# Performance work log

Hardware: AMD Instinct MI355X
Metric: run time of the kernel (lower is better)

## Reference

```python
import jax, jax.numpy as jnp
import numpy as np

EPS = 1e-5

def conv2d(x, w, b=None, pad=1):
    # x: [B,C,H,W], w: [O,I,kh,kw]
    y = jax.lax.conv_general_dilated(x, w, (1, 1), [(pad, pad), (pad, pad)],
                                     dimension_numbers=('NCHW', 'OIHW', 'NCHW'))
    if b is not None:
        y = y + b[None, :, None, None]
    return y

def bn(x, g, b, m, v):
    # inference-mode batchnorm
    inv = g / jnp.sqrt(v + EPS)
    return x * inv[None, :, None, None] + (b - m * inv)[None, :, None, None]

def coord_conv(x, w, b):
    B, C, H, W = x.shape
    yy = jnp.broadcast_to(jnp.linspace(-1.0, 1.0, H)[:, None], (H, W))
    xx = jnp.broadcast_to(jnp.linspace(-1.0, 1.0, W)[None, :], (H, W))
    coords = jnp.broadcast_to(jnp.stack([xx, yy])[None], (B, 2, H, W)).astype(x.dtype)
    return conv2d(jnp.concatenate([x, coords], axis=1), w, b, pad=1)

def deform_conv(x, offset, w):
    # deformable conv v1, 3x3, pad=1, stride=1, no bias
    B, C, H, W = x.shape
    K = 9
    # offset channels interleaved (y, x) per kernel tap
    off = offset.reshape(B, K, 2, H, W)
    off_y, off_x = off[:, :, 0], off[:, :, 1]          # [B,9,H,W]
    k = jnp.arange(K)
    ko_y = (k // 3 - 1).astype(x.dtype)[None, :, None, None]
    ko_x = (k % 3 - 1).astype(x.dtype)[None, :, None, None]
    base_y = jnp.arange(H, dtype=x.dtype)[None, None, :, None]
    base_x = jnp.arange(W, dtype=x.dtype)[None, None, None, :]
    py = base_y + ko_y + off_y                          # [B,9,H,W]
    px = base_x + ko_x + off_x
    xf = x.reshape(B, C, H * W)
    y0 = jnp.floor(py)
    x0 = jnp.floor(px)
    acc = jnp.zeros((B, C, K, H, W), x.dtype)
    for dy in (0.0, 1.0):
        for dx in (0.0, 1.0):
            yy = y0 + dy
            xx = x0 + dx
            wgt = (1.0 - jnp.abs(py - yy)) * (1.0 - jnp.abs(px - xx))
            valid = (yy >= 0) & (yy < H) & (xx >= 0) & (xx < W)
            wgt = jnp.where(valid, wgt, 0.0)            # zero padding OOB
            yi = jnp.clip(yy, 0, H - 1).astype(jnp.int32)
            xi = jnp.clip(xx, 0, W - 1).astype(jnp.int32)
            idx = (yi * W + xi).reshape(B, K * H * W)
            v = jnp.take_along_axis(xf, idx[:, None, :], axis=2).reshape(B, C, K, H, W)
            acc = acc + v * wgt[:, None]
    wk = w.reshape(w.shape[0], w.shape[1], K)           # [O,I,9]
    return jnp.einsum('bckhw,ock->bohw', acc, wk)

def setup_inputs() -> dict:
    key = jax.random.key(0)
    ks = jax.random.split(key, 16)
    d_model, hd = 256, 64
    B, H, W = 8, 96, 96
    f32 = jnp.float32
    def bn_params(k):
        k1, k2, k3 = jax.random.split(k, 3)
        return (1.0 + 0.1 * jax.random.normal(k1, (hd,), f32),
                0.1 * jax.random.normal(k2, (hd,), f32),
                0.1 * jax.random.normal(k3, (hd,), f32),
                0.5 + jax.random.uniform(jax.random.fold_in(k, 7), (hd,), f32))
    bn1 = bn_params(ks[1]); bn2 = bn_params(ks[2]); bn3 = bn_params(ks[3]); bn4 = bn_params(ks[4])
    inp = {
        'features': jax.random.normal(ks[0], (B, H, W, d_model), f32),
        'coord_w': 0.05 * jax.random.normal(ks[5], (hd, d_model + 2, 3, 3), f32),
        'coord_b': jnp.zeros((hd,), f32),
        'bn1_g': bn1[0], 'bn1_b': bn1[1], 'bn1_m': bn1[2], 'bn1_v': bn1[3],
        'off_w': 0.01 * jax.random.normal(ks[6], (18, hd, 3, 3), f32),
        'off_b': 0.01 * jax.random.normal(ks[7], (18,), f32),
        'dc_w': 0.05 * jax.random.normal(ks[8], (hd, hd, 3, 3), f32),
        'bn2_g': bn2[0], 'bn2_b': bn2[1], 'bn2_m': bn2[2], 'bn2_v': bn2[3],
        'r1_w': 0.05 * jax.random.normal(ks[9], (hd, hd, 3, 3), f32),
        'bn3_g': bn3[0], 'bn3_b': bn3[1], 'bn3_m': bn3[2], 'bn3_v': bn3[3],
        'r2_w': 0.05 * jax.random.normal(ks[10], (hd, hd, 3, 3), f32),
        'bn4_g': bn4[0], 'bn4_b': bn4[1], 'bn4_m': bn4[2], 'bn4_v': bn4[3],
        'out_w': 0.1 * jax.random.normal(ks[11], (1, hd, 1, 1), f32),
        'out_b': jnp.zeros((1,), f32),
    }
    return inp

def reference(features, coord_w, coord_b, bn1_g, bn1_b, bn1_m, bn1_v,
              off_w, off_b, dc_w, bn2_g, bn2_b, bn2_m, bn2_v,
              r1_w, bn3_g, bn3_b, bn3_m, bn3_v,
              r2_w, bn4_g, bn4_b, bn4_m, bn4_v, out_w, out_b):
    x = jnp.transpose(features, (0, 3, 1, 2))           # NHWC -> NCHW
    x = jax.nn.relu(bn(coord_conv(x, coord_w, coord_b), bn1_g, bn1_b, bn1_m, bn1_v))
    offset = conv2d(x, off_w, off_b, pad=1)
    x = deform_conv(x, offset, dc_w)
    x = jax.nn.relu(bn(x, bn2_g, bn2_b, bn2_m, bn2_v))
    x = jax.nn.relu(bn(conv2d(x, r1_w, None, pad=1), bn3_g, bn3_b, bn3_m, bn3_v))
    x = jax.nn.relu(bn(conv2d(x, r2_w, None, pad=1), bn4_g, bn4_b, bn4_m, bn4_v))
    return jax.nn.sigmoid(conv2d(x, out_w, out_b, pad=0))
```

## Files before the change

### kernel.cpp

```cpp
#include <hip/hip_runtime.h>


typedef unsigned short u16;
typedef unsigned int u32;
typedef __attribute__((ext_vector_type(8)))  short bf16x8;
typedef __attribute__((ext_vector_type(16))) float f32x16;

#define EPSBN 1e-5f

__device__ __forceinline__ u16 f2bf(float f) {
  u32 u = __builtin_bit_cast(u32, f);
  u32 r = u + 0x7FFFu + ((u >> 16) & 1u);
  return (u16)(r >> 16);
}
__device__ __forceinline__ u32 pk2(float a, float b) {
  return (u32)f2bf(a) | ((u32)f2bf(b) << 16);
}
__device__ __forceinline__ float lo2f(u32 w) { return __builtin_bit_cast(float, w << 16); }
__device__ __forceinline__ float hi2f(u32 w) { return __builtin_bit_cast(float, w & 0xFFFF0000u); }

#define N_WCF 147456
#define N_WCC 9216
#define N_WOF 18432
#define N_W64 36864
#define N_ALLW (N_WCF + N_WCC + N_WOF + 3*N_W64)

__global__ __launch_bounds__(256) void prep_kernel(
    const float* __restrict__ coord_w, const float* __restrict__ off_w,
    const float* __restrict__ dc_w, const float* __restrict__ r1_w,
    const float* __restrict__ r2_w,
    u16* __restrict__ wcf, u16* __restrict__ wcc, u16* __restrict__ wof,
    u16* __restrict__ wdf, u16* __restrict__ wr1, u16* __restrict__ wr2)
{
  int i = blockIdx.x * 256 + threadIdx.x;
  if (i >= N_ALLW) return;
  int d = i;
  if (d < N_WCF) {
    int j = d & 7, lane = (d >> 3) & 63, frag = d >> 9;
    int nt = frag & 1, h = (frag >> 1) & 3, tap = (frag >> 3) % 9, cc = (frag >> 3) / 9;
    int ic = cc * 64 + h * 16 + ((lane >> 5) << 3) + j;
    int oc = nt * 32 + (lane & 31);
    wcf[d] = f2bf(coord_w[((size_t)oc * 258 + ic) * 9 + tap]);
    return;
  }
  d -= N_WCF;
  if (d < N_WCC) {
    int j = d & 7, lane = (d >> 3) & 63, frag = d >> 9;
    int nt = frag & 1, tap = frag >> 1;
    int ic = 256 + ((lane >> 5) << 3) + j;
    int oc = nt * 32 + (lane & 31);
    wcc[d] = (ic < 258) ? f2bf(coord_w[((size_t)oc * 258 + ic) * 9 + tap]) : (u16)0;
    return;
  }
  d -= N_WCC;
  if (d < N_WOF) {
    int j = d & 7, lane = (d >> 3) & 63, frag = d >> 9;
    int h = frag & 3, tap = frag >> 2;
    int ic = h * 16 + ((lane >> 5) << 3) + j;
    int oc = lane & 31;
    wof[d] = (oc < 18) ? f2bf(off_w[((size_t)oc * 64 + ic) * 9 + tap]) : (u16)0;
    return;
  }
  d -= N_WOF;
  int seg = d / N_W64;
  int e = d - seg * N_W64;
  int j = e & 7, lane = (e >> 3) & 63, frag = e >> 9;
  int nt = frag & 1, h = (frag >> 1) & 3, tap = frag >> 3;
  int ic = h * 16 + ((lane >> 5) << 3) + j;
  int oc = nt * 32 + (lane & 31);
  const float* src = (seg == 0) ? dc_w : (seg == 1) ? r1_w : r2_w;
  u16* dst = (seg == 0) ? wdf : (seg == 1) ? wr1 : wr2;
  dst[e] = f2bf(src[((size_t)oc * 64 + ic) * 9 + tap]);
}

__global__ __launch_bounds__(512, 2) void coord_conv_kernel(
    const float* __restrict__ feat, const u16* __restrict__ wcf,
    const u16* __restrict__ wcc, const float* __restrict__ cb,
    const float* __restrict__ g, const float* __restrict__ bb,
    const float* __restrict__ m, const float* __restrict__ v,
    u16* __restrict__ x1b)
{
  __shared__ __align__(16) u16 tile[6 * 34 * 72];
  const int t = threadIdx.x;
  const int wv = t >> 6, lane = t & 63;
  const int l31 = lane & 31, l5 = lane >> 5;
  const int rp = wv & 1, ntw = (wv >> 1) & 1, kh = wv >> 2;
  const int x0 = blockIdx.x * 32, y0 = blockIdx.y * 4, b = blockIdx.z;

  f32x16 acc[2] = {};
  float4 pa[4], pb[4];
  bf16x8 wfr[18];

  auto issueF = [&](int cc) {
    #pragma unroll
    for (int r = 0; r < 4; ++r) {
      const int i = t + r * 512;
      const float4 z = {0.f, 0.f, 0.f, 0.f};
      pa[r] = z; pb[r] = z;
      if (i < 1632) {
        const int px = i >> 3, gg = i & 7;
        const int ly = px / 34, lx = px - ly * 34;
        const int gy = y0 + ly - 1, gx = x0 + lx - 1;
        if ((unsigned)gy < 96u && (unsigned)gx < 96u) {
          const float* p = feat + ((size_t)((b * 96 + gy) * 96 + gx)) * 256
                           + cc * 64 + gg * 8;
          pa[r] = *(const float4*)p;
          pb[r] = *(const float4*)(p + 4);
        }
      }
    }
  };
  auto commitF = [&]() {
    #pragma unroll
    for (int r = 0; r < 4; ++r) {
      const int i = t + r * 512;
      if (i < 1632) {
        const int px = i >> 3, gg = i & 7;
        uint4 o;
        o.x = pk2(pa[r].x, pa[r].y); o.y = pk2(pa[r].z, pa[r].w);
        o.z = pk2(pb[r].x, pb[r].y); o.w = pk2(pb[r].z, pb[r].w);
        *(uint4*)(tile + px * 72 + gg * 8) = o;
      }
    }
  };
  auto loadW = [&](int cc) {
    #pragma unroll
    for (int tap = 0; tap < 9; ++tap)
      #pragma unroll
      for (int hh = 0; hh < 2; ++hh) {
        const int h = kh * 2 + hh;
        wfr[tap * 2 + hh] = *(const bf16x8*)(wcf +
            ((size_t)((((cc * 9 + tap) * 4 + h) * 2) + ntw)) * 512 + lane * 8);
      }
  };

  issueF(0);
  loadW(0);
  for (int cc = 0; cc < 4; ++cc) {
    __syncthreads();
    commitF();
    __syncthreads();
    if (cc < 3) issueF(cc + 1);
    #pragma unroll
    for (int tap = 0; tap < 9; ++tap) {
      const int dy = tap / 3, dx = tap - dy * 3;
      #pragma unroll
      for (int hh = 0; hh < 2; ++hh) {
        const bf16x8 bfr = wfr[tap * 2 + hh];
        #pragma unroll
        for (int ai = 0; ai < 2; ++ai) {
          const bf16x8 afr = *(const bf16x8*)(tile +
              ((rp * 2 + ai + dy) * 34 + l31 + dx) * 72
              + (kh * 2 + hh) * 16 + l5 * 8);
          acc[ai] = __builtin_amdgcn_mfma_f32_32x32x16_bf16(afr, bfr, acc[ai],
                                                            0, 0, 0);
        }
      }
    }
    if (cc < 3) loadW(cc + 1);
  }

  bf16x8 wcr[9];
  if (kh == 0) {
    #pragma unroll
    for (int tap = 0; tap < 9; ++tap)
      wcr[tap] = *(const bf16x8*)(wcc + ((size_t)(tap * 2 + ntw)) * 512
                                  + lane * 8);
  }
  __syncthreads();
  for (int i = t; i < 408; i += 512) {
    const int px = i >> 1, gg = i & 1;
    const int ly = px / 34, lx = px - ly * 34;
    const int gy = y0 + ly - 1, gx = x0 + lx - 1;
    uint4 o = {0u, 0u, 0u, 0u};
    if (gg == 0 && (unsigned)gy < 96u && (unsigned)gx < 96u) {
      const float xx = -1.f + (2.f / 95.f) * (float)gx;
      const float yy = -1.f + (2.f / 95.f) * (float)gy;
      o.x = pk2(xx, yy);
    }
    *(uint4*)(tile + (ly * 34 + lx) * 72 + gg * 8) = o;
  }
  __syncthreads();
  if (kh == 0) {
    #pragma unroll
    for (int tap = 0; tap < 9; ++tap) {
      const int dy = tap / 3, dx = tap - dy * 3;
      #pragma unroll
      for (int ai = 0; ai < 2; ++ai) {
        const bf16x8 afr = *(const bf16x8*)(tile +
            ((rp * 2 + ai + dy) * 34 + l31 + dx) * 72 + l5 * 8);
        acc[ai] = __builtin_amdgcn_mfma_f32_32x32x16_bf16(afr, wcr[tap],
                                                          acc[ai], 0, 0, 0);
      }
    }
  }

  float* redk = (float*)tile;
  const int slot = wv & 3;
  #pragma unroll
  for (int ai = 0; ai < 2; ++ai) {
    __syncthreads();
    if (kh == 1) {
      #pragma unroll
      for (int r = 0; r < 16; ++r)
        redk[(r * 4 + slot) * 64 + lane] = acc[ai][r];
    }
    __syncthreads();
    if (kh == 0) {
      #pragma unroll
      for (int r = 0; r < 16; ++r)
        acc[ai][r] += redk[(r * 4 + slot) * 64 + lane];
    }
  }

  if (kh == 0) {
    const int oc = ntw * 32 + l31;
    const float inv = g[oc] * rsqrtf(v[oc] + EPSBN);
    const float sh = bb[oc] - m[oc] * inv + cb[oc] * inv;
    #pragma unroll
    for (int ai = 0; ai < 2; ++ai) {
      const int y = y0 + rp * 2 + ai;
      #pragma unroll
      for (int r = 0; r < 16; ++r) {
        const int xr = (r & 3) + 8 * (r >> 2) + 4 * l5;
        const float val = fmaxf(fmaf(acc[ai][r], inv, sh), 0.f);
        x1b[((size_t)((b * 96 + y) * 96 + x0 + xr)) * 64 + oc] = f2bf(val);
      }
    }
  }
}

template<int NN, int EPI>
__global__ __launch_bounds__(512, 2) void conv64_kernel(
    const u16* __restrict__ xin, const u16* __restrict__ wf,
    const float* __restrict__ bias,
    const float* __restrict__ g, const float* __restrict__ bb,
    const float* __restrict__ m, const float* __restrict__ v,
    const float* __restrict__ ow, const float* __restrict__ ob,
    void* __restrict__ outp)
{
  __shared__ __align__(16) u16 tile[6 * 34 * 72];
  __shared__ float red2[2][128];
  const int t = threadIdx.x;
  const int wv = t >> 6, lane = t & 63;
  const int l31 = lane & 31, l5 = lane >> 5;
  const int rp  = (NN == 2) ? (wv & 1) : 0;
  const int ntw = (NN == 2) ? ((wv >> 1) & 1) : 0;
  const int row = (NN == 2) ? 0 : (wv & 3);
  const int kh  = wv >> 2;
  const int x0 = blockIdx.x * 32, y0 = blockIdx.y * 4, b = blockIdx.z;

  uint4 pf[4];
  #pragma unroll
  for (int r = 0; r < 4; ++r) {
    const int i = t + r * 512;
    const uint4 z = {0u, 0u, 0u, 0u};
    pf[r] = z;
    if (i < 1632) {
      const int px = i >> 3, gg = i & 7;
      const int ly = px / 34, lx = px - ly * 34;
      const int gy = y0 + ly - 1, gx = x0 + lx - 1;
      if ((unsigned)gy < 96u && (unsigned)gx < 96u)
        pf[r] = *(const uint4*)(xin + (((size_t)((b * 96 + gy) * 96 + gx)) << 6)
                                + gg * 8);
    }
  }
  bf16x8 wfr[18];
  #pragma unroll
  for (int tap = 0; tap < 9; ++tap)
    #pragma unroll
    for (int hh = 0; hh < 2; ++hh) {
      const int h = kh * 2 + hh;
      const size_t f = (NN == 2) ? (size_t)((tap * 4 + h) * 2 + ntw)
                                 : (size_t)(tap * 4 + h);
      wfr[tap * 2 + hh] = *(const bf16x8*)(wf + f * 512 + lane * 8);
    }
  #pragma unroll
  for (int r = 0; r < 4; ++r) {
    const int i = t + r * 512;
    if (i < 1632) {
      const int px = i >> 3, gg = i & 7;
      *(uint4*)(tile + px * 72 + gg * 8) = pf[r];
    }
  }
  __syncthreads();

  constexpr int NA = (NN == 2) ? 2 : 1;
  f32x16 acc[NA] = {};
  #pragma unroll
  for (int tap = 0; tap < 9; ++tap) {
    const int dy = tap / 3, dx = tap - dy * 3;
    #pragma unroll
    for (int hh = 0; hh < 2; ++hh) {
      const int h = kh * 2 + hh;
      #pragma unroll
      for (int ai = 0; ai < NA; ++ai) {
        const int rr = (NN == 2) ? (rp * 2 + ai) : row;
        const bf16x8 afr = *(const bf16x8*)(tile +
            ((rr + dy) * 34 + l31 + dx) * 72 + h * 16 + l5 * 8);
        acc[ai] = __builtin_amdgcn_mfma_f32_32x32x16_bf16(afr, wfr[tap * 2 + hh],
                                                          acc[ai], 0, 0, 0);
      }
    }
  }

  float* redk = (float*)tile;
  const int slot = (NN == 2) ? (wv & 3) : row;
  #pragma unroll
  for (int ai = 0; ai < NA; ++ai) {
    __syncthreads();
    if (kh == 1) {
      #pragma unroll
      for (int r = 0; r < 16; ++r)
        redk[(r * 4 + slot) * 64 + lane] = acc[ai][r];
    }
    __syncthreads();
    if (kh == 0) {
      #pragma unroll
      for (int r = 0; r < 16; ++r)
        acc[ai][r] += redk[(r * 4 + slot) * 64 + lane];
    }
  }

  if constexpr (EPI == 0) {
    if (kh == 0) {
      u16* xo = (u16*)outp;
      const int oc = ntw * 32 + l31;
      const float inv = g[oc] * rsqrtf(v[oc] + EPSBN);
      const float sh = bb[oc] - m[oc] * inv;
      #pragma unroll
      for (int ai = 0; ai < NA; ++ai) {
        const int y = y0 + rp * 2 + ai;
        #pragma unroll
        for (int r = 0; r < 16; ++r) {
          const int xr = (r & 3) + 8 * (r >> 2) + 4 * l5;
          const float val = fmaxf(fmaf(acc[ai][r], inv, sh), 0.f);
          xo[((size_t)((b * 96 + y) * 96 + x0 + xr)) * 64 + oc] = f2bf(val);
        }
      }
    }
  } else if constexpr (EPI == 1) {
    if (kh == 0 && l31 < 18) {
      float* fo = (float*)outp;
      const int y = y0 + row;
      const float bs = bias[l31];
      #pragma unroll
      for (int r = 0; r < 16; ++r) {
        const int xr = (r & 3) + 8 * (r >> 2) + 4 * l5;
        fo[((size_t)((b * 96 + y) * 96 + x0 + xr)) * 18 + l31] = acc[0][r] + bs;
      }
    }
  } else {
    if (kh == 0) {
      const int oc = ntw * 32 + l31;
      const float inv = g[oc] * rsqrtf(v[oc] + EPSBN);
      const float sh = bb[oc] - m[oc] * inv;
      const float wo = ow[oc];
      #pragma unroll
      for (int ai = 0; ai < NA; ++ai) {
        float pr[16];
        #pragma unroll
        for (int r = 0; r < 16; ++r) {
          const float val = fmaxf(fmaf(acc[ai][r], inv, sh), 0.f);
          pr[r] = val * wo;
        }
        #pragma unroll
        for (int mask = 1; mask <= 16; mask <<= 1)
          #pragma unroll
          for (int r = 0; r < 16; ++r)
            pr[r] += __shfl_xor(pr[r], mask);
        if (l31 == 0) {
          #pragma unroll
          for (int r = 0; r < 16; ++r) {
            const int xr = (r & 3) + 8 * (r >> 2) + 4 * l5;
            red2[ntw][(rp * 2 + ai) * 32 + xr] = pr[r];
          }
        }
      }
    }
    __syncthreads();
    if (t < 128) {
      float* fo = (float*)outp;
      const int yy = y0 + (t >> 5), xx = x0 + (t & 31);
      const float val = red2[0][t] + red2[1][t] + ob[0];
      fo[(size_t)(b * 96 + yy) * 96 + xx] = 1.f / (1.f + expf(-val));
    }
  }
}

__global__ __launch_bounds__(512, 4) void deform_kernel(
    const u16* __restrict__ x1b, const float* __restrict__ off,
    const u16* __restrict__ wdf,
    const float* __restrict__ g, const float* __restrict__ bb,
    const float* __restrict__ m, const float* __restrict__ v,
    u16* __restrict__ x2b)
{
  __shared__ __align__(16) u16 s[2 * 128 * 72];
  __shared__ float offs[128 * 18];
  const int t = threadIdx.x;
  const int wv = t >> 6, lane = t & 63;
  const int l31 = lane & 31, l5 = lane >> 5;
  const int mt = wv & 3, ntw = wv >> 2;
  const int x0 = blockIdx.x * 16, y0 = blockIdx.y * 8, b = blockIdx.z;

  {
    float po[5];
    #pragma unroll
    for (int r = 0; r < 5; ++r) {
      const int i = t + r * 512;
      po[r] = 0.f;
      if (i < 2304) {
        const int p = i / 18, c = i - p * 18;
        const int gy = y0 + (p >> 4), gx = x0 + (p & 15);
        po[r] = off[((size_t)((b * 96 + gy) * 96 + gx)) * 18 + c];
      }
    }
    #pragma unroll
    for (int r = 0; r < 5; ++r) {
      const int i = t + r * 512;
      if (i < 2304) offs[i] = po[r];
    }
  }
  __syncthreads();

  const int sp = t >> 2, part = t & 3;
  const int sy = y0 + (sp >> 4), sx = x0 + (sp & 15);

  uint4 gbuf[8];
  float w4[4];

  auto prefetch = [&](int k) {
    const float oy = offs[sp * 18 + 2 * k];
    const float ox = offs[sp * 18 + 2 * k + 1];
    const float py = (float)(sy + k / 3 - 1) + oy;
    const float px = (float)(sx + k % 3 - 1) + ox;
    const float yf = floorf(py), xf = floorf(px);
    const float fy = py - yf, fx = px - xf;
    const int yi = (int)yf, xi = (int)xf;
    #pragma unroll
    for (int cor = 0; cor < 4; ++cor) {
      const int cy = yi + (cor >> 1), cx = xi + (cor & 1);
      const uint4 z = {0u, 0u, 0u, 0u};
      gbuf[2 * cor] = z; gbuf[2 * cor + 1] = z;
      const float wy = (cor & 2) ? fy : 1.f - fy;
      const float wx = (cor & 1) ? fx : 1.f - fx;
      w4[cor] = 0.f;
      if ((unsigned)cy < 96u && (unsigned)cx < 96u) {
        w4[cor] = wy * wx;
        const u16* p = x1b + ((size_t)((b * 96 + cy) * 96 + cx)) * 64
                       + part * 16;
        gbuf[2 * cor]     = *(const uint4*)p;
        gbuf[2 * cor + 1] = *(const uint4*)(p + 8);
      }
    }
  };
  auto combine = [&](u16* dst) {
    float val[16];
    #pragma unroll
    for (int j = 0; j < 16; ++j) val[j] = 0.f;
    #pragma unroll
    for (int cor = 0; cor < 4; ++cor) {
      const float wgt = w4[cor];
      const u32 uu[8] = {gbuf[2 * cor].x, gbuf[2 * cor].y,
                         gbuf[2 * cor].z, gbuf[2 * cor].w,
                         gbuf[2 * cor + 1].x, gbuf[2 * cor + 1].y,
                         gbuf[2 * cor + 1].z, gbuf[2 * cor + 1].w};
      #pragma unroll
      for (int u = 0; u < 8; ++u) {
        val[2 * u]     = fmaf(wgt, lo2f(uu[u]), val[2 * u]);
        val[2 * u + 1] = fmaf(wgt, hi2f(uu[u]), val[2 * u + 1]);
      }
    }
    u32 pk[8];
    #pragma unroll
    for (int u = 0; u < 8; ++u) pk[u] = pk2(val[2 * u], val[2 * u + 1]);
    uint4 w0 = {pk[0], pk[1], pk[2], pk[3]};
    uint4 w1 = {pk[4], pk[5], pk[6], pk[7]};
    *(uint4*)(dst + sp * 72 + part * 16) = w0;
    *(uint4*)(dst + sp * 72 + part * 16 + 8) = w1;
  };

  f32x16 acc = {};

  prefetch(0);
  combine(s);
  __syncthreads();

  for (int k = 0; k < 9; ++k) {
    u16* cur = s + (k & 1) * 9216;
    if (k < 8) prefetch(k + 1);
    #pragma unroll
    for (int h = 0; h < 4; ++h) {
      const bf16x8 afr = *(const bf16x8*)(cur + (mt * 32 + l31) * 72
                                          + h * 16 + l5 * 8);
      const bf16x8 bfr = *(const bf16x8*)(wdf +
          ((size_t)((k * 4 + h) * 2 + ntw)) * 512 + lane * 8);
      acc = __builtin_amdgcn_mfma_f32_32x32x16_bf16(afr, bfr, acc, 0, 0, 0);
    }
    if (k < 8) combine(s + ((k + 1) & 1) * 9216);
    __syncthreads();
  }

  const int oc = ntw * 32 + l31;
  const float inv = g[oc] * rsqrtf(v[oc] + EPSBN);
  const float sh = bb[oc] - m[oc] * inv;
  #pragma unroll
  for (int r = 0; r < 16; ++r) {
    const int pxi = mt * 32 + (r & 3) + 8 * (r >> 2) + 4 * l5;
    const int y = y0 + (pxi >> 4), x = x0 + (pxi & 15);
    const float val = fmaxf(fmaf(acc[r], inv, sh), 0.f);
    x2b[((size_t)((b * 96 + y) * 96 + x)) * 64 + oc] = f2bf(val);
  }
}

extern "C" void kernel_launch(void* const* d_in, const int* in_sizes, int n_in,
                              void* d_out, int out_size, void* d_ws,
                              size_t ws_size, hipStream_t stream)
{
  (void)in_sizes; (void)n_in; (void)out_size; (void)ws_size;
  const float* features = (const float*)d_in[0];
  const float* coord_w  = (const float*)d_in[1];
  const float* coord_b  = (const float*)d_in[2];
  const float* bn1g = (const float*)d_in[3];
  const float* bn1b = (const float*)d_in[4];
  const float* bn1m = (const float*)d_in[5];
  const float* bn1v = (const float*)d_in[6];
  const float* off_w = (const float*)d_in[7];
  const float* off_b = (const float*)d_in[8];
  const float* dc_w  = (const float*)d_in[9];
  const float* bn2g = (const float*)d_in[10];
  const float* bn2b = (const float*)d_in[11];
  const float* bn2m = (const float*)d_in[12];
  const float* bn2v = (const float*)d_in[13];
  const float* r1_w = (const float*)d_in[14];
  const float* bn3g = (const float*)d_in[15];
  const float* bn3b = (const float*)d_in[16];
  const float* bn3m = (const float*)d_in[17];
  const float* bn3v = (const float*)d_in[18];
  const float* r2_w = (const float*)d_in[19];
  const float* bn4g = (const float*)d_in[20];
  const float* bn4b = (const float*)d_in[21];
  const float* bn4m = (const float*)d_in[22];
  const float* bn4v = (const float*)d_in[23];
  const float* out_w = (const float*)d_in[24];
  const float* out_b = (const float*)d_in[25];

  char* W = (char*)d_ws;
  float* offb = (float*)W;
  u16*   x1b  = (u16*)(W + 5308416);
  u16*   x2b  = (u16*)(W + 14745600);
  u16*   x3b  = (u16*)(W + 24182784);
  u16*   wcf  = (u16*)(W + 33619968);
  u16*   wcc  = wcf + N_WCF;
  u16*   wof  = wcc + N_WCC;
  u16*   wdf  = wof + N_WOF;
  u16*   wr1  = wdf + N_W64;
  u16*   wr2  = wr1 + N_W64;

  prep_kernel<<<(N_ALLW + 255) / 256, 256, 0, stream>>>(
      coord_w, off_w, dc_w, r1_w, r2_w, wcf, wcc, wof, wdf, wr1, wr2);

  dim3 grid(3, 24, 8);
  dim3 gridD(6, 12, 8);

  coord_conv_kernel<<<grid, 512, 0, stream>>>(
      features, wcf, wcc, coord_b, bn1g, bn1b, bn1m, bn1v, x1b);
  conv64_kernel<1, 1><<<grid, 512, 0, stream>>>(
      x1b, wof, off_b, nullptr, nullptr, nullptr, nullptr, nullptr, nullptr,
      (void*)offb);
  deform_kernel<<<gridD, 512, 0, stream>>>(
      x1b, offb, wdf, bn2g, bn2b, bn2m, bn2v, x2b);
  conv64_kernel<2, 0><<<grid, 512, 0, stream>>>(
      x2b, wr1, nullptr, bn3g, bn3b, bn3m, bn3v, nullptr, nullptr, (void*)x3b);
  conv64_kernel<2, 2><<<grid, 512, 0, stream>>>(
      x3b, wr2, nullptr, bn4g, bn4b, bn4m, bn4v, out_w, out_b, d_out);
}
```

Baseline: 251.0 us.

## Fuse offset conv into deform kernel and fuse the two residual convs

The offset conv is now computed inside the deformable-conv kernel from a haloed x1 tile in shared memory, so the fp32 offset tensor is never written to or read from global memory. The two trailing 3x3 convs plus the 1x1 sigmoid head are merged into one kernel that recomputes the first conv over a halo region and keeps the intermediate in LDS, which drops the x3 round trip and two launches. In exchange, halo pixels are computed redundantly, LDS use per block rises (which may lower occupancy), and the deform kernel's launch bound drops from 4 to 2 blocks.

```diff
diff --git a/kernel.cpp b/kernel.cpp
--- a/kernel.cpp
+++ b/kernel.cpp
@@ -230,199 +230,95 @@
   }
 }
 
-template<int NN, int EPI>
-__global__ __launch_bounds__(512, 2) void conv64_kernel(
-    const u16* __restrict__ xin, const u16* __restrict__ wf,
-    const float* __restrict__ bias,
-    const float* __restrict__ g, const float* __restrict__ bb,
-    const float* __restrict__ m, const float* __restrict__ v,
-    const float* __restrict__ ow, const float* __restrict__ ob,
-    void* __restrict__ outp)
-{
-  __shared__ __align__(16) u16 tile[6 * 34 * 72];
-  __shared__ float red2[2][128];
-  const int t = threadIdx.x;
-  const int wv = t >> 6, lane = t & 63;
-  const int l31 = lane & 31, l5 = lane >> 5;
-  const int rp  = (NN == 2) ? (wv & 1) : 0;
-  const int ntw = (NN == 2) ? ((wv >> 1) & 1) : 0;
-  const int row = (NN == 2) ? 0 : (wv & 3);
-  const int kh  = wv >> 2;
-  const int x0 = blockIdx.x * 32, y0 = blockIdx.y * 4, b = blockIdx.z;
-
-  uint4 pf[4];
-  #pragma unroll
-  for (int r = 0; r < 4; ++r) {
-    const int i = t + r * 512;
-    const uint4 z = {0u, 0u, 0u, 0u};
-    pf[r] = z;
-    if (i < 1632) {
-      const int px = i >> 3, gg = i & 7;
-      const int ly = px / 34, lx = px - ly * 34;
-      const int gy = y0 + ly - 1, gx = x0 + lx - 1;
-      if ((unsigned)gy < 96u && (unsigned)gx < 96u)
-        pf[r] = *(const uint4*)(xin + (((size_t)((b * 96 + gy) * 96 + gx)) << 6)
-                                + gg * 8);
-    }
-  }
-  bf16x8 wfr[18];
-  #pragma unroll
-  for (int tap = 0; tap < 9; ++tap)
-    #pragma unroll
-    for (int hh = 0; hh < 2; ++hh) {
-      const int h = kh * 2 + hh;
-      const size_t f = (NN == 2) ? (size_t)((tap * 4 + h) * 2 + ntw)
-                                 : (size_t)(tap * 4 + h);
-      wfr[tap * 2 + hh] = *(const bf16x8*)(wf + f * 512 + lane * 8);
-    }
-  #pragma unroll
-  for (int r = 0; r < 4; ++r) {
-    const int i = t + r * 512;
-    if (i < 1632) {
-      const int px = i >> 3, gg = i & 7;
-      *(uint4*)(tile + px * 72 + gg * 8) = pf[r];
-    }
-  }
-  __syncthreads();
-
-  constexpr int NA = (NN == 2) ? 2 : 1;
-  f32x16 acc[NA] = {};
-  #pragma unroll
-  for (int tap = 0; tap < 9; ++tap) {
-    const int dy = tap / 3, dx = tap - dy * 3;
-    #pragma unroll
-    for (int hh = 0; hh < 2; ++hh) {
-      const int h = kh * 2 + hh;
-      #pragma unroll
-      for (int ai = 0; ai < NA; ++ai) {
-        const int rr = (NN == 2) ? (rp * 2 + ai) : row;
-        const bf16x8 afr = *(const bf16x8*)(tile +
-            ((rr + dy) * 34 + l31 + dx) * 72 + h * 16 + l5 * 8);
-        acc[ai] = __builtin_amdgcn_mfma_f32_32x32x16_bf16(afr, wfr[tap * 2 + hh],
-                                                          acc[ai], 0, 0, 0);
-      }
-    }
-  }
-
-  float* redk = (float*)tile;
-  const int slot = (NN == 2) ? (wv & 3) : row;
-  #pragma unroll
-  for (int ai = 0; ai < NA; ++ai) {
-    __syncthreads();
-    if (kh == 1) {
-      #pragma unroll
-      for (int r = 0; r < 16; ++r)
-        redk[(r * 4 + slot) * 64 + lane] = acc[ai][r];
-    }
-    __syncthreads();
-    if (kh == 0) {
-      #pragma unroll
-      for (int r = 0; r < 16; ++r)
-        acc[ai][r] += redk[(r * 4 + slot) * 64 + lane];
-    }
-  }
-
-  if constexpr (EPI == 0) {
-    if (kh == 0) {
-      u16* xo = (u16*)outp;
-      const int oc = ntw * 32 + l31;
-      const float inv = g[oc] * rsqrtf(v[oc] + EPSBN);
-      const float sh = bb[oc] - m[oc] * inv;
-      #pragma unroll
-      for (int ai = 0; ai < NA; ++ai) {
-        const int y = y0 + rp * 2 + ai;
-        #pragma unroll
-        for (int r = 0; r < 16; ++r) {
-          const int xr = (r & 3) + 8 * (r >> 2) + 4 * l5;
-          const float val = fmaxf(fmaf(acc[ai][r], inv, sh), 0.f);
-          xo[((size_t)((b * 96 + y) * 96 + x0 + xr)) * 64 + oc] = f2bf(val);
-        }
-      }
-    }
-  } else if constexpr (EPI == 1) {
-    if (kh == 0 && l31 < 18) {
-      float* fo = (float*)outp;
-      const int y = y0 + row;
-      const float bs = bias[l31];
-      #pragma unroll
-      for (int r = 0; r < 16; ++r) {
-        const int xr = (r & 3) + 8 * (r >> 2) + 4 * l5;
-        fo[((size_t)((b * 96 + y) * 96 + x0 + xr)) * 18 + l31] = acc[0][r] + bs;
-      }
-    }
-  } else {
-    if (kh == 0) {
-      const int oc = ntw * 32 + l31;
-      const float inv = g[oc] * rsqrtf(v[oc] + EPSBN);
-      const float sh = bb[oc] - m[oc] * inv;
-      const float wo = ow[oc];
-      #pragma unroll
-      for (int ai = 0; ai < NA; ++ai) {
-        float pr[16];
-        #pragma unroll
-        for (int r = 0; r < 16; ++r) {
-          const float val = fmaxf(fmaf(acc[ai][r], inv, sh), 0.f);
-          pr[r] = val * wo;
-        }
-        #pragma unroll
-        for (int mask = 1; mask <= 16; mask <<= 1)
-          #pragma unroll
-          for (int r = 0; r < 16; ++r)
-            pr[r] += __shfl_xor(pr[r], mask);
-        if (l31 == 0) {
-          #pragma unroll
-          for (int r = 0; r < 16; ++r) {
-            const int xr = (r & 3) + 8 * (r >> 2) + 4 * l5;
-            red2[ntw][(rp * 2 + ai) * 32 + xr] = pr[r];
-          }
-        }
-      }
-    }
-    __syncthreads();
-    if (t < 128) {
-      float* fo = (float*)outp;
-      const int yy = y0 + (t >> 5), xx = x0 + (t & 31);
-      const float val = red2[0][t] + red2[1][t] + ob[0];
-      fo[(size_t)(b * 96 + yy) * 96 + xx] = 1.f / (1.f + expf(-val));
-    }
-  }
-}
-
-__global__ __launch_bounds__(512, 4) void deform_kernel(
-    const u16* __restrict__ x1b, const float* __restrict__ off,
-    const u16* __restrict__ wdf,
+__global__ __launch_bounds__(512, 2) void deform_fused_kernel(
+    const u16* __restrict__ x1b, const u16* __restrict__ wof,
+    const float* __restrict__ offb_bias, const u16* __restrict__ wdf,
     const float* __restrict__ g, const float* __restrict__ bb,
     const float* __restrict__ m, const float* __restrict__ v,
     u16* __restrict__ x2b)
 {
+  __shared__ __align__(16) u16 xt[180 * 72];
   __shared__ __align__(16) u16 s[2 * 128 * 72];
   __shared__ float offs[128 * 18];
   const int t = threadIdx.x;
   const int wv = t >> 6, lane = t & 63;
   const int l31 = lane & 31, l5 = lane >> 5;
+  const int x0 = blockIdx.x * 16, y0 = blockIdx.y * 8, b = blockIdx.z;
+
+  {
+    uint4 pf[3];
+    #pragma unroll
+    for (int rr = 0; rr < 3; ++rr) {
+      const int i = t + rr * 512;
+      const uint4 z = {0u, 0u, 0u, 0u};
+      pf[rr] = z;
+      if (i < 1440) {
+        const int px = i >> 3, part = i & 7;
+        const int ly = px / 18, lx = px - ly * 18;
+        const int gy = y0 + ly - 1, gx = x0 + lx - 1;
+        if ((unsigned)gy < 96u && (unsigned)gx < 96u)
+          pf[rr] = *(const uint4*)(x1b +
+              (((size_t)((b * 96 + gy) * 96 + gx)) << 6) + part * 8);
+      }
+    }
+    #pragma unroll
+    for (int rr = 0; rr < 3; ++rr) {
+      const int i = t + rr * 512;
+      if (i < 1440) {
+        const int px = i >> 3, part = i & 7;
+        *(uint4*)(xt + px * 72 + part * 8) = pf[rr];
+      }
+    }
+  }
+  __syncthreads();
+
+  {
+    const int mt = wv & 3, kh = wv >> 2;
+    bf16x8 wfr[18];
+    #pragma unroll
+    for (int tap = 0; tap < 9; ++tap)
+      #pragma unroll
+      for (int hh = 0; hh < 2; ++hh)
+        wfr[tap * 2 + hh] = *(const bf16x8*)(wof +
+            ((size_t)(tap * 4 + kh * 2 + hh)) * 512 + lane * 8);
+    const int px = mt * 32 + l31;
+    const int r = px >> 4, c = px & 15;
+    f32x16 acc = {};
+    #pragma unroll
+    for (int tap = 0; tap < 9; ++tap) {
+      const int dy = tap / 3, dx = tap - dy * 3;
+      #pragma unroll
+      for (int hh = 0; hh < 2; ++hh) {
+        const bf16x8 a = *(const bf16x8*)(xt +
+            ((r + dy) * 18 + c + dx) * 72 + (kh * 2 + hh) * 16 + l5 * 8);
+        acc = __builtin_amdgcn_mfma_f32_32x32x16_bf16(a, wfr[tap * 2 + hh],
+                                                      acc, 0, 0, 0);
+      }
+    }
+    float* redk = (float*)s;
+    if (kh == 1) {
+      #pragma unroll
+      for (int r2 = 0; r2 < 16; ++r2)
+        redk[(mt * 16 + r2) * 64 + lane] = acc[r2];
+    }
+    __syncthreads();
+    if (kh == 0) {
+      #pragma unroll
+      for (int r2 = 0; r2 < 16; ++r2)
+        acc[r2] += redk[(mt * 16 + r2) * 64 + lane];
+      if (l31 < 18) {
+        const float bs = offb_bias[l31];
+        #pragma unroll
+        for (int r2 = 0; r2 < 16; ++r2) {
+          const int opx = mt * 32 + (r2 & 3) + 8 * (r2 >> 2) + 4 * l5;
+          offs[opx * 18 + l31] = acc[r2] + bs;
+        }
+      }
+    }
+  }
+  __syncthreads();
+
   const int mt = wv & 3, ntw = wv >> 2;
-  const int x0 = blockIdx.x * 16, y0 = blockIdx.y * 8, b = blockIdx.z;
-
-  {
-    float po[5];
-    #pragma unroll
-    for (int r = 0; r < 5; ++r) {
-      const int i = t + r * 512;
-      po[r] = 0.f;
-      if (i < 2304) {
-        const int p = i / 18, c = i - p * 18;
-        const int gy = y0 + (p >> 4), gx = x0 + (p & 15);
-        po[r] = off[((size_t)((b * 96 + gy) * 96 + gx)) * 18 + c];
-      }
-    }
-    #pragma unroll
-    for (int r = 0; r < 5; ++r) {
-      const int i = t + r * 512;
-      if (i < 2304) offs[i] = po[r];
-    }
-  }
-  __syncthreads();
-
   const int sp = t >> 2, part = t & 3;
   const int sy = y0 + (sp >> 4), sx = x0 + (sp & 15);
 
@@ -510,6 +406,179 @@
     const int y = y0 + (pxi >> 4), x = x0 + (pxi & 15);
     const float val = fmaxf(fmaf(acc[r], inv, sh), 0.f);
     x2b[((size_t)((b * 96 + y) * 96 + x)) * 64 + oc] = f2bf(val);
+  }
+}
+
+__global__ __launch_bounds__(512, 2) void tail_fused_kernel(
+    const u16* __restrict__ x2b, const u16* __restrict__ wr1,
+    const u16* __restrict__ wr2,
+    const float* __restrict__ g3, const float* __restrict__ b3,
+    const float* __restrict__ m3, const float* __restrict__ v3,
+    const float* __restrict__ g4, const float* __restrict__ b4,
+    const float* __restrict__ m4, const float* __restrict__ v4,
+    const float* __restrict__ ow, const float* __restrict__ ob,
+    float* __restrict__ outp)
+{
+  __shared__ __align__(16) u16 xt2[288 * 72];
+  __shared__ __align__(16) u16 xt3[204 * 72];
+  __shared__ float red2[2][128];
+  const int t = threadIdx.x;
+  const int wv = t >> 6, lane = t & 63;
+  const int l31 = lane & 31, l5 = lane >> 5;
+  const int x0 = blockIdx.x * 32, y0 = blockIdx.y * 4, b = blockIdx.z;
+
+  {
+    uint4 pf[5];
+    #pragma unroll
+    for (int rr = 0; rr < 5; ++rr) {
+      const int i = t + rr * 512;
+      const uint4 z = {0u, 0u, 0u, 0u};
+      pf[rr] = z;
+      if (i < 2304) {
+        const int px = i >> 3, part = i & 7;
+        const int ly = px / 36, lx = px - ly * 36;
+        const int gy = y0 + ly - 2, gx = x0 + lx - 2;
+        if ((unsigned)gy < 96u && (unsigned)gx < 96u)
+          pf[rr] = *(const uint4*)(x2b +
+              (((size_t)((b * 96 + gy) * 96 + gx)) << 6) + part * 8);
+      }
+    }
+    #pragma unroll
+    for (int rr = 0; rr < 5; ++rr) {
+      const int i = t + rr * 512;
+      if (i < 2304) {
+        const int px = i >> 3, part = i & 7;
+        *(uint4*)(xt2 + px * 72 + part * 8) = pf[rr];
+      }
+    }
+  }
+  __syncthreads();
+
+  {
+    const int nt = wv & 1, ms = wv >> 1;
+    const int m1 = ms + 4;
+    const bool has1 = (m1 < 7);
+    const int pxc0 = min(ms * 32 + l31, 203);
+    const int ly0 = pxc0 / 34, lx0 = pxc0 - ly0 * 34;
+    const int pxc1 = min(m1 * 32 + l31, 203);
+    const int ly1 = pxc1 / 34, lx1 = pxc1 - ly1 * 34;
+    f32x16 a0 = {}, a1 = {};
+    #pragma unroll
+    for (int tap = 0; tap < 9; ++tap) {
+      const int dy = tap / 3, dx = tap - dy * 3;
+      #pragma unroll
+      for (int h = 0; h < 4; ++h) {
+        const bf16x8 wf = *(const bf16x8*)(wr1 +
+            ((size_t)((tap * 4 + h) * 2 + nt)) * 512 + lane * 8);
+        const bf16x8 f0 = *(const bf16x8*)(xt2 +
+            ((ly0 + dy) * 36 + lx0 + dx) * 72 + h * 16 + l5 * 8);
+        a0 = __builtin_amdgcn_mfma_f32_32x32x16_bf16(f0, wf, a0, 0, 0, 0);
+        if (has1) {
+          const bf16x8 f1 = *(const bf16x8*)(xt2 +
+              ((ly1 + dy) * 36 + lx1 + dx) * 72 + h * 16 + l5 * 8);
+          a1 = __builtin_amdgcn_mfma_f32_32x32x16_bf16(f1, wf, a1, 0, 0, 0);
+        }
+      }
+    }
+    const int oc = nt * 32 + l31;
+    const float inv = g3[oc] * rsqrtf(v3[oc] + EPSBN);
+    const float sh = b3[oc] - m3[oc] * inv;
+    #pragma unroll
+    for (int r = 0; r < 16; ++r) {
+      const int xr = (r & 3) + 8 * (r >> 2) + 4 * l5;
+      const int p0 = ms * 32 + xr;
+      if (p0 < 204) {
+        const int ly = p0 / 34, lx = p0 - ly * 34;
+        const int gy = y0 + ly - 1, gx = x0 + lx - 1;
+        const bool in0 = ((unsigned)gy < 96u) && ((unsigned)gx < 96u);
+        xt3[p0 * 72 + oc] =
+            in0 ? f2bf(fmaxf(fmaf(a0[r], inv, sh), 0.f)) : (u16)0;
+      }
+      if (has1) {
+        const int p1 = m1 * 32 + xr;
+        if (p1 < 204) {
+          const int ly = p1 / 34, lx = p1 - ly * 34;
+          const int gy = y0 + ly - 1, gx = x0 + lx - 1;
+          const bool in1 = ((unsigned)gy < 96u) && ((unsigned)gx < 96u);
+          xt3[p1 * 72 + oc] =
+              in1 ? f2bf(fmaxf(fmaf(a1[r], inv, sh), 0.f)) : (u16)0;
+        }
+      }
+    }
+  }
+  __syncthreads();
+
+  {
+    const int rp = wv & 1, ntw = (wv >> 1) & 1, kh = wv >> 2;
+    bf16x8 wfr[18];
+    #pragma unroll
+    for (int tap = 0; tap < 9; ++tap)
+      #pragma unroll
+      for (int hh = 0; hh < 2; ++hh)
+        wfr[tap * 2 + hh] = *(const bf16x8*)(wr2 +
+            ((size_t)((tap * 4 + kh * 2 + hh) * 2 + ntw)) * 512 + lane * 8);
+    f32x16 acc[2] = {};
+    #pragma unroll
+    for (int tap = 0; tap < 9; ++tap) {
+      const int dy = tap / 3, dx = tap - dy * 3;
+      #pragma unroll
+      for (int hh = 0; hh < 2; ++hh) {
+        const bf16x8 bfr = wfr[tap * 2 + hh];
+        #pragma unroll
+        for (int ai = 0; ai < 2; ++ai) {
+          const bf16x8 a = *(const bf16x8*)(xt3 +
+              ((rp * 2 + ai + dy) * 34 + l31 + dx) * 72
+              + (kh * 2 + hh) * 16 + l5 * 8);
+          acc[ai] = __builtin_amdgcn_mfma_f32_32x32x16_bf16(a, bfr, acc[ai],
+                                                            0, 0, 0);
+        }
+      }
+    }
+    float* redk = (float*)xt2;
+    __syncthreads();
+    if (kh == 1) {
+      #pragma unroll
+      for (int ai = 0; ai < 2; ++ai)
+        #pragma unroll
+        for (int r = 0; r < 16; ++r)
+          redk[(((rp * 2 + ai) * 2 + ntw) * 16 + r) * 64 + lane] = acc[ai][r];
+    }
+    __syncthreads();
+    if (kh == 0) {
+      const int oc = ntw * 32 + l31;
+      const float inv = g4[oc] * rsqrtf(v4[oc] + EPSBN);
+      const float sh = b4[oc] - m4[oc] * inv;
+      const float wo = ow[oc];
+      #pragma unroll
+      for (int ai = 0; ai < 2; ++ai) {
+        float pr[16];
+        #pragma unroll
+        for (int r = 0; r < 16; ++r) {
+          const float a = acc[ai][r] +
+              redk[(((rp * 2 + ai) * 2 + ntw) * 16 + r) * 64 + lane];
+          const float val = fmaxf(fmaf(a, inv, sh), 0.f);
+          pr[r] = val * wo;
+        }
+        #pragma unroll
+        for (int mask = 1; mask <= 16; mask <<= 1)
+          #pragma unroll
+          for (int r = 0; r < 16; ++r)
+            pr[r] += __shfl_xor(pr[r], mask);
+        if (l31 == 0) {
+          #pragma unroll
+          for (int r = 0; r < 16; ++r) {
+            const int xr = (r & 3) + 8 * (r >> 2) + 4 * l5;
+            red2[ntw][(rp * 2 + ai) * 32 + xr] = pr[r];
+          }
+        }
+      }
+    }
+    __syncthreads();
+    if (t < 128) {
+      const int yy = y0 + (t >> 5), xx = x0 + (t & 31);
+      const float val = red2[0][t] + red2[1][t] + ob[0];
+      outp[(size_t)(b * 96 + yy) * 96 + xx] = 1.f / (1.f + expf(-val));
+    }
   }
 }
 
@@ -546,16 +615,14 @@
   const float* out_b = (const float*)d_in[25];
 
   char* W = (char*)d_ws;
-  float* offb = (float*)W;
-  u16*   x1b  = (u16*)(W + 5308416);
-  u16*   x2b  = (u16*)(W + 14745600);
-  u16*   x3b  = (u16*)(W + 24182784);
-  u16*   wcf  = (u16*)(W + 33619968);
-  u16*   wcc  = wcf + N_WCF;
-  u16*   wof  = wcc + N_WCC;
-  u16*   wdf  = wof + N_WOF;
-  u16*   wr1  = wdf + N_W64;
-  u16*   wr2  = wr1 + N_W64;
+  u16* x1b = (u16*)W;
+  u16* x2b = (u16*)(W + 9437184);
+  u16* wcf = (u16*)(W + 18874368);
+  u16* wcc = wcf + N_WCF;
+  u16* wof = wcc + N_WCC;
+  u16* wdf = wof + N_WOF;
+  u16* wr1 = wdf + N_W64;
+  u16* wr2 = wr1 + N_W64;
 
   prep_kernel<<<(N_ALLW + 255) / 256, 256, 0, stream>>>(
       coord_w, off_w, dc_w, r1_w, r2_w, wcf, wcc, wof, wdf, wr1, wr2);
@@ -565,13 +632,9 @@
 
   coord_conv_kernel<<<grid, 512, 0, stream>>>(
       features, wcf, wcc, coord_b, bn1g, bn1b, bn1m, bn1v, x1b);
-  conv64_kernel<1, 1><<<grid, 512, 0, stream>>>(
-      x1b, wof, off_b, nullptr, nullptr, nullptr, nullptr, nullptr, nullptr,
-      (void*)offb);
-  deform_kernel<<<gridD, 512, 0, stream>>>(
-      x1b, offb, wdf, bn2g, bn2b, bn2m, bn2v, x2b);
-  conv64_kernel<2, 0><<<grid, 512, 0, stream>>>(
-      x2b, wr1, nullptr, bn3g, bn3b, bn3m, bn3v, nullptr, nullptr, (void*)x3b);
-  conv64_kernel<2, 2><<<grid, 512, 0, stream>>>(
-      x3b, wr2, nullptr, bn4g, bn4b, bn4m, bn4v, out_w, out_b, d_out);
+  deform_fused_kernel<<<gridD, 512, 0, stream>>>(
+      x1b, wof, off_b, wdf, bn2g, bn2b, bn2m, bn2v, x2b);
+  tail_fused_kernel<<<grid, 512, 0, stream>>>(
+      x2b, wr1, wr2, bn3g, bn3b, bn3m, bn3v,
+      bn4g, bn4b, bn4m, bn4v, out_w, out_b, (float*)d_out);
 }
```

Result: slower. 258.2 us (+2.9%).
